# Kernel tuning notes

Hardware: AMD Instinct MI355X
Metric: run time of the kernel (lower is better)

Reference implementation:

```python
import jax, jax.numpy as jnp
import numpy as np

TEMPERATURE = 0.2

def setup_inputs() -> dict:
    key = jax.random.key(0)
    k1, k2 = jax.random.split(key)
    B, D = 4096, 128
    emb_i = jax.random.normal(k1, (B, D), dtype=jnp.float32)
    emb_j = jax.random.normal(k2, (B, D), dtype=jnp.float32)
    return {"emb_i": emb_i, "emb_j": emb_j}

def reference(emb_i, emb_j):
    # L2-normalize each embedding row, concat -> z: [2B, D]
    z_i = emb_i / jnp.linalg.norm(emb_i, axis=1, keepdims=True)
    z_j = emb_j / jnp.linalg.norm(emb_j, axis=1, keepdims=True)
    z = jnp.concatenate([z_i, z_j], axis=0)          # [2B, D]
    N2 = z.shape[0]
    N = N2 // 2
    # cosine similarity of normalized vectors == dot product
    sim = z @ z.T                                    # [2B, 2B]
    logits = sim / TEMPERATURE
    # denominator excludes only the diagonal (k != i)
    diag_mask = jnp.eye(N2, dtype=bool)
    masked = jnp.where(diag_mask, -jnp.inf, logits)
    lse = jax.nn.logsumexp(masked, axis=1)           # [2B]
    # positive pair for row i is i+N (mod 2N)
    pos_idx = jnp.concatenate([jnp.arange(N) + N, jnp.arange(N)])
    pos_logits = jnp.take_along_axis(logits, pos_idx[:, None], axis=1)[:, 0]
    # loss = (1/2N) * sum_i -log( exp(pos_i) / sum_{k!=i} exp(logits[i,k]) )
    loss = jnp.mean(lse - pos_logits)
    return loss
```

## Files before the change

kernel.cpp:

```cpp
#include <hip/hip_runtime.h>
#include <hip/hip_bf16.h>

typedef __attribute__((ext_vector_type(8))) short bf16x8;
typedef __attribute__((ext_vector_type(4))) float f32x4;

#define EXP_SCALE 7.213475204444817f

__device__ __forceinline__ float fast_exp2(float x) {
#if __has_builtin(__builtin_amdgcn_exp2f)
  return __builtin_amdgcn_exp2f(x);
#else
  return exp2f(x);
#endif
}

__device__ __forceinline__ unsigned short f32_to_bf16(float f) {
  unsigned int u = __float_as_uint(f);
  unsigned int r = (u + 0x7FFFu + ((u >> 16) & 1u)) >> 16;
  return (unsigned short)r;
}


__global__ __launch_bounds__(256) void k_normalize(
    const float* __restrict__ emb_i, const float* __restrict__ emb_j,
    unsigned short* __restrict__ z, float* __restrict__ out)
{
  if (blockIdx.x == 0 && threadIdx.x == 0) out[0] = 0.0f;
  const int w = threadIdx.x >> 6;
  const int lane = threadIdx.x & 63;
  const int row = (blockIdx.x << 2) + w;
  const float* src = (row < 4096) ? (emb_i + row * 128) : (emb_j + (row - 4096) * 128);
  float2 v = reinterpret_cast<const float2*>(src)[lane];
  float ss = v.x * v.x + v.y * v.y;
  #pragma unroll
  for (int m = 1; m < 64; m <<= 1) ss += __shfl_xor(ss, m, 64);
  float rinv = 1.0f / sqrtf(ss);
  ushort2 st;
  st.x = f32_to_bf16(v.x * rinv);
  st.y = f32_to_bf16(v.y * rinv);
  const int e = lane << 1;
  const int kk = e >> 5;
  const int q = (e >> 3) & 3;
  const int rem = e & 7;
  const int tile = row >> 4;
  const int c = row & 15;
  unsigned short* dst = z + tile * 2048 + kk * 512 + ((q << 4) + c) * 8 + rem;
  *reinterpret_cast<ushort2*>(dst) = st;
}

__global__ __launch_bounds__(256, 2) void k_simlse(
    const unsigned short* __restrict__ z,
    float* __restrict__ rowsum,
    float* __restrict__ rowpos)
{
  const int w = threadIdx.x >> 6;
  const int lane = threadIdx.x & 63;
  const int q = lane >> 4;
  const int c = lane & 15;
  const int rb = blockIdx.x >> 3;
  const int ch = blockIdx.x & 7;
  const int R0 = rb << 7;

  __shared__ short smem[16384];
  {
    const unsigned short* zA = z + (R0 >> 4) * 2048;
    #pragma unroll
    for (int j = 0; j < 8; ++j) {
      const int v = (j << 8) + threadIdx.x;
      *reinterpret_cast<bf16x8*>(&smem[v << 3]) =
          *reinterpret_cast<const bf16x8*>(zA + (v << 3));
    }
  }
  __syncthreads();
  bf16x8 a[8][4];
  #pragma unroll
  for (int rg = 0; rg < 8; ++rg)
    #pragma unroll
    for (int kk = 0; kk < 4; ++kk)
      a[rg][kk] = *reinterpret_cast<const bf16x8*>(
          &smem[rg * 2048 + kk * 512 + (lane << 3)]);

  float acc[8][4];
  #pragma unroll
  for (int rg = 0; rg < 8; ++rg)
    #pragma unroll
    for (int e = 0; e < 4; ++e) acc[rg][e] = 0.0f;
  float pacc[2][4] = {{0.f,0.f,0.f,0.f},{0.f,0.f,0.f,0.f}};

  const int ct0 = (ch << 6) + w;
  const int pos0 = ((R0 + 4096) & 8191) >> 4;
  const int ipb = ((pos0 >> 6) == ch) ? ((pos0 & 63) >> 2) : -99;

  const unsigned short* bwave = z + ct0 * 2048 + (lane << 3);

  bf16x8 b0[4], b1[4];
  auto ldb = [&](bf16x8 (&dst)[4], int idx) {
    const unsigned short* p = bwave + idx * 8192;
    dst[0] = *reinterpret_cast<const bf16x8*>(p);
    dst[1] = *reinterpret_cast<const bf16x8*>(p + 512);
    dst[2] = *reinterpret_cast<const bf16x8*>(p + 1024);
    dst[3] = *reinterpret_cast<const bf16x8*>(p + 1536);
  };

  auto process = [&](const bf16x8 (&bb)[4], int i) {
    #pragma unroll
    for (int hb = 0; hb < 2; ++hb) {
      f32x4 cc[4];
      #pragma unroll
      for (int rr = 0; rr < 4; ++rr) cc[rr] = f32x4{0.f, 0.f, 0.f, 0.f};
      #pragma unroll
      for (int kk = 0; kk < 4; ++kk)
        #pragma unroll
        for (int rr = 0; rr < 4; ++rr)
          cc[rr] = __builtin_amdgcn_mfma_f32_16x16x32_bf16(
              a[(hb << 2) + rr][kk], bb[kk], cc[rr], 0, 0, 0);
      #pragma unroll
      for (int rr = 0; rr < 4; ++rr)
        #pragma unroll
        for (int e = 0; e < 4; ++e)
          acc[(hb << 2) + rr][e] +=
              fast_exp2(__builtin_fmaf(cc[rr][e], EXP_SCALE, -EXP_SCALE));
      if (i == ipb + hb) {
        #pragma unroll
        for (int rr = 0; rr < 4; ++rr) {
          if (rr == w) {
            #pragma unroll
            for (int e = 0; e < 4; ++e)
              if (c == ((q << 2) + e)) pacc[hb][e] = cc[rr][e] * 5.0f;
          }
        }
      }
    }
  };

  ldb(b0, 0);
  #pragma unroll 1
  for (int i = 0; i < 16; i += 2) {
    ldb(b1, i + 1);
    process(b0, i);
    if (i + 2 < 16) ldb(b0, i + 2);
    process(b1, i + 1);
  }

  #pragma unroll
  for (int m = 1; m < 16; m <<= 1) {
    #pragma unroll
    for (int rg = 0; rg < 8; ++rg)
      #pragma unroll
      for (int e = 0; e < 4; ++e)
        acc[rg][e] += __shfl_xor(acc[rg][e], m, 64);
    #pragma unroll
    for (int hb = 0; hb < 2; ++hb)
      #pragma unroll
      for (int e = 0; e < 4; ++e)
        pacc[hb][e] += __shfl_xor(pacc[hb][e], m, 64);
  }

  __shared__ float lsum[4 * 128];
  __shared__ float lpos[4 * 32];
  __syncthreads();
  if (c == 0) {
    #pragma unroll
    for (int rg = 0; rg < 8; ++rg)
      #pragma unroll
      for (int e = 0; e < 4; ++e)
        lsum[w * 128 + rg * 16 + (q << 2) + e] = acc[rg][e];
    #pragma unroll
    for (int hb = 0; hb < 2; ++hb)
      #pragma unroll
      for (int e = 0; e < 4; ++e)
        lpos[w * 32 + hb * 16 + (q << 2) + e] = pacc[hb][e];
  }
  __syncthreads();
  if (threadIdx.x < 128) {
    const int t = threadIdx.x;
    const int r = R0 + t;
    float s = lsum[t] + lsum[128 + t] + lsum[256 + t] + lsum[384 + t];
    rowsum[(ch << 13) + r] = s;
    if (ch == (pos0 >> 6)) {
      const int rg = t >> 4;
      rowpos[r] = lpos[(rg & 3) * 32 + (rg >> 2) * 16 + (t & 15)];
    }
  }
}

__global__ __launch_bounds__(256) void k_finish(
    const float* __restrict__ rowsum, const float* __restrict__ rowpos,
    float* __restrict__ out)
{
  const int r = blockIdx.x * 256 + threadIdx.x;
  float tot = -1.0f;
  #pragma unroll
  for (int chunk = 0; chunk < 8; ++chunk) tot += rowsum[(chunk << 13) + r];
  float v = 5.0f + logf(tot) - rowpos[r];
  #pragma unroll
  for (int m = 1; m < 64; m <<= 1) v += __shfl_xor(v, m, 64);
  __shared__ float red[4];
  if ((threadIdx.x & 63) == 0) red[threadIdx.x >> 6] = v;
  __syncthreads();
  if (threadIdx.x == 0)
    atomicAdd(out, (red[0] + red[1] + red[2] + red[3]) * (1.0f / 8192.0f));
}

extern "C" void kernel_launch(void* const* d_in, const int* in_sizes, int n_in,
                              void* d_out, int out_size, void* d_ws, size_t ws_size,
                              hipStream_t stream) {
  const float* emb_i = (const float*)d_in[0];
  const float* emb_j = (const float*)d_in[1];
  unsigned short* z = (unsigned short*)d_ws;
  float* rowsum = (float*)((char*)d_ws + 8192 * 128 * 2);
  float* rowpos = rowsum + 8 * 8192;
  float* out = (float*)d_out;

  k_normalize<<<2048, 256, 0, stream>>>(emb_i, emb_j, z, out);
  k_simlse<<<512, 256, 0, stream>>>(z, rowsum, rowpos);
  k_finish<<<32, 256, 0, stream>>>(rowsum, rowpos, out);
}
```

Measured before the change: 88.64 us.

## Exploit similarity matrix symmetry to compute only upper-triangular tiles

Since z·zᵀ is symmetric, the grid now covers only the upper-triangular (row block, column chunk) tiles. It uses a triangular block index and narrower 512-column chunks. Off-diagonal tiles also reduce their exp values along columns and atomically add them into the transposed rows' sums. Positive logits are stored once and reused for both halves, and the per-chunk rowsum buffer becomes a single atomically accumulated array zeroed in the normalize kernel. This roughly halves the MFMA and exp work. The cost is extra shuffles, shared-memory column reductions and global float atomics, which make the summation order nondeterministic.

```diff
diff --git a/kernel.cpp b/kernel.cpp
--- a/kernel.cpp
+++ b/kernel.cpp
@@ -23,9 +23,11 @@
 
 __global__ __launch_bounds__(256) void k_normalize(
     const float* __restrict__ emb_i, const float* __restrict__ emb_j,
-    unsigned short* __restrict__ z, float* __restrict__ out)
+    unsigned short* __restrict__ z, float* __restrict__ rowsum,
+    float* __restrict__ out)
 {
   if (blockIdx.x == 0 && threadIdx.x == 0) out[0] = 0.0f;
+  if (threadIdx.x < 4) rowsum[(blockIdx.x << 2) + threadIdx.x] = 0.0f;
   const int w = threadIdx.x >> 6;
   const int lane = threadIdx.x & 63;
   const int row = (blockIdx.x << 2) + w;
@@ -57,9 +59,15 @@
   const int lane = threadIdx.x & 63;
   const int q = lane >> 4;
   const int c = lane & 15;
-  const int rb = blockIdx.x >> 3;
-  const int ch = blockIdx.x & 7;
+
+  int ch = 0;
+  {
+    const int b = blockIdx.x;
+    while (b >= 2 * (ch + 1) * (ch + 2)) ++ch;
+  }
+  const int rb = blockIdx.x - 2 * ch * (ch + 1);
   const int R0 = rb << 7;
+  const bool upper = (rb < (ch << 2));
 
   __shared__ short smem[16384];
   {
@@ -87,11 +95,15 @@
     for (int e = 0; e < 4; ++e) acc[rg][e] = 0.0f;
   float pacc[2][4] = {{0.f,0.f,0.f,0.f},{0.f,0.f,0.f,0.f}};
 
-  const int ct0 = (ch << 6) + w;
-  const int pos0 = ((R0 + 4096) & 8191) >> 4;
-  const int ipb = ((pos0 >> 6) == ch) ? ((pos0 & 63) >> 2) : -99;
-
+  __shared__ float colacc[512];
+  __shared__ float lsum[4 * 128];
+  __shared__ float lpos[4 * 32];
+
+  const int ct0 = (ch << 5) + w;
   const unsigned short* bwave = z + ct0 * 2048 + (lane << 3);
+
+  const int pos0t = ((R0 + 4096) & 8191) >> 4;
+  const int ipb = ((pos0t >> 5) == ch) ? ((pos0t & 31) >> 2) : -99;
 
   bf16x8 b0[4], b1[4];
   auto ldb = [&](bf16x8 (&dst)[4], int idx) {
@@ -103,6 +115,7 @@
   };
 
   auto process = [&](const bf16x8 (&bb)[4], int i) {
+    float colp = 0.0f;
     #pragma unroll
     for (int hb = 0; hb < 2; ++hb) {
       f32x4 cc[4];
@@ -117,9 +130,11 @@
       #pragma unroll
       for (int rr = 0; rr < 4; ++rr)
         #pragma unroll
-        for (int e = 0; e < 4; ++e)
-          acc[(hb << 2) + rr][e] +=
-              fast_exp2(__builtin_fmaf(cc[rr][e], EXP_SCALE, -EXP_SCALE));
+        for (int e = 0; e < 4; ++e) {
+          float t = fast_exp2(__builtin_fmaf(cc[rr][e], EXP_SCALE, -EXP_SCALE));
+          acc[(hb << 2) + rr][e] += t;
+          if (upper) colp += t;
+        }
       if (i == ipb + hb) {
         #pragma unroll
         for (int rr = 0; rr < 4; ++rr) {
@@ -131,14 +146,20 @@
         }
       }
     }
+    if (upper) {
+      colp += __shfl_xor(colp, 16, 64);
+      colp += __shfl_xor(colp, 32, 64);
+      if (lane < 16)
+        colacc[(((i << 2) + w) << 4) + c] = colp;
+    }
   };
 
   ldb(b0, 0);
   #pragma unroll 1
-  for (int i = 0; i < 16; i += 2) {
+  for (int i = 0; i < 8; i += 2) {
     ldb(b1, i + 1);
     process(b0, i);
-    if (i + 2 < 16) ldb(b0, i + 2);
+    if (i + 2 < 8) ldb(b0, i + 2);
     process(b1, i + 1);
   }
 
@@ -156,30 +177,35 @@
         pacc[hb][e] += __shfl_xor(pacc[hb][e], m, 64);
   }
 
-  __shared__ float lsum[4 * 128];
-  __shared__ float lpos[4 * 32];
+  if (c == 0) {
+    #pragma unroll
+    for (int rg = 0; rg < 8; ++rg)
+      #pragma unroll
+      for (int e = 0; e < 4; ++e)
+        lsum[w * 128 + rg * 16 + (q << 2) + e] = acc[rg][e];
+    #pragma unroll
+    for (int hb = 0; hb < 2; ++hb)
+      #pragma unroll
+      for (int e = 0; e < 4; ++e)
+        lpos[w * 32 + hb * 16 + (q << 2) + e] = pacc[hb][e];
+  }
   __syncthreads();
-  if (c == 0) {
-    #pragma unroll
-    for (int rg = 0; rg < 8; ++rg)
-      #pragma unroll
-      for (int e = 0; e < 4; ++e)
-        lsum[w * 128 + rg * 16 + (q << 2) + e] = acc[rg][e];
-    #pragma unroll
-    for (int hb = 0; hb < 2; ++hb)
-      #pragma unroll
-      for (int e = 0; e < 4; ++e)
-        lpos[w * 32 + hb * 16 + (q << 2) + e] = pacc[hb][e];
-  }
-  __syncthreads();
+
   if (threadIdx.x < 128) {
     const int t = threadIdx.x;
     const int r = R0 + t;
     float s = lsum[t] + lsum[128 + t] + lsum[256 + t] + lsum[384 + t];
-    rowsum[(ch << 13) + r] = s;
-    if (ch == (pos0 >> 6)) {
+    atomicAdd(&rowsum[r], s);
+    if (ipb != -99) {
       const int rg = t >> 4;
       rowpos[r] = lpos[(rg & 3) * 32 + (rg >> 2) * 16 + (t & 15)];
+    }
+  }
+  if (upper) {
+    #pragma unroll
+    for (int j = 0; j < 2; ++j) {
+      const int idx = (j << 8) + threadIdx.x;
+      atomicAdd(&rowsum[(ch << 9) + idx], colacc[idx]);
     }
   }
 }
@@ -189,10 +215,8 @@
     float* __restrict__ out)
 {
   const int r = blockIdx.x * 256 + threadIdx.x;
-  float tot = -1.0f;
-  #pragma unroll
-  for (int chunk = 0; chunk < 8; ++chunk) tot += rowsum[(chunk << 13) + r];
-  float v = 5.0f + logf(tot) - rowpos[r];
+  float tot = rowsum[r] - 1.0f;
+  float v = 5.0f + logf(tot) - rowpos[r & 4095];
   #pragma unroll
   for (int m = 1; m < 64; m <<= 1) v += __shfl_xor(v, m, 64);
   __shared__ float red[4];
@@ -209,10 +233,10 @@
   const float* emb_j = (const float*)d_in[1];
   unsigned short* z = (unsigned short*)d_ws;
   float* rowsum = (float*)((char*)d_ws + 8192 * 128 * 2);
-  float* rowpos = rowsum + 8 * 8192;
+  float* rowpos = rowsum + 8192;
   float* out = (float*)d_out;
 
-  k_normalize<<<2048, 256, 0, stream>>>(emb_i, emb_j, z, out);
-  k_simlse<<<512, 256, 0, stream>>>(z, rowsum, rowpos);
+  k_normalize<<<2048, 256, 0, stream>>>(emb_i, emb_j, z, rowsum, out);
+  k_simlse<<<544, 256, 0, stream>>>(z, rowsum, rowpos);
   k_finish<<<32, 256, 0, stream>>>(rowsum, rowpos, out);
 }
```

After: 89.36 us. About the same (+0.8%).
